# Optimization experiments

Measured on AMD Instinct MI355X. Metric: run time of the kernel, lower is better.

Reference implementation:

```python
import jax, jax.numpy as jnp
import numpy as np

EMBED = 768
HEADS = 12
HEAD_DIM = EMBED // HEADS
B, S = 1, 4096


def setup_inputs() -> dict:
    key = jax.random.key(0)
    ks = jax.random.split(key, 8)
    values = jax.random.normal(ks[0], (B, S, EMBED), dtype=jnp.float32)
    keys_in = jax.random.normal(ks[1], (B, S, EMBED), dtype=jnp.float32)
    queries = jax.random.normal(ks[2], (B, S, EMBED), dtype=jnp.float32)
    # causal mask: 1.0 where attention is disallowed (gets * -1e9)
    mask = jnp.triu(jnp.ones((S, S), dtype=jnp.float32), k=1)[None, None, :, :]
    sc = 1.0 / np.sqrt(EMBED)
    W_q = jax.random.normal(ks[3], (EMBED, EMBED), dtype=jnp.float32) * sc
    W_k = jax.random.normal(ks[4], (EMBED, EMBED), dtype=jnp.float32) * sc
    W_v = jax.random.normal(ks[5], (EMBED, EMBED), dtype=jnp.float32) * sc
    W_o = jax.random.normal(ks[6], (EMBED, EMBED), dtype=jnp.float32) * sc
    b_o = jnp.zeros((EMBED,), dtype=jnp.float32)
    return {"values": values, "keys": keys_in, "queries": queries, "mask": mask,
            "W_q": W_q, "W_k": W_k, "W_v": W_v, "W_o": W_o, "b_o": b_o}


def reference(values, keys, queries, mask, W_q, W_k, W_v, W_o, b_o):
    N, S_, _ = queries.shape
    # linear projections (Dense, no bias)
    q = queries @ W_q  # [N, S, E]
    k = keys @ W_k
    v = values @ W_v
    # split heads -> [N, H, S, Dh]
    def split(x):
        return x.reshape(N, S_, HEADS, HEAD_DIM).transpose(0, 2, 1, 3)
    q, k, v = split(q), split(k), split(v)
    scores = jnp.einsum('nhqd,nhkd->nhqk', q, k) / jnp.sqrt(
        jnp.asarray(HEAD_DIM, dtype=q.dtype))
    scores = scores + mask * (-1e9)
    attn = jax.nn.softmax(scores, axis=-1)
    out = jnp.einsum('nhqk,nhkd->nhqd', attn, v)  # [N, H, S, Dh]
    out = out.transpose(0, 2, 1, 3).reshape(N, S_, EMBED)
    return out @ W_o + b_o
```

## Files before the change

kernel.cpp:

```cpp
#include <hip/hip_runtime.h>

#define S_LEN 4096
#define EMB   768
#define NH    12
#define DH    64

typedef __attribute__((ext_vector_type(8))) short bf16x8;
typedef __attribute__((ext_vector_type(4))) float f32x4;

__device__ __forceinline__ unsigned short f2bf(float f) {
    union { float f; unsigned u; } v; v.f = f;
    unsigned r = v.u + 0x7fffu + ((v.u >> 16) & 1u);
    return (unsigned short)(r >> 16);
}
__device__ __forceinline__ float bf2f(unsigned short u) {
    union { unsigned u; float f; } v; v.u = (unsigned)u << 16; return v.f;
}
__device__ __forceinline__ unsigned pk2(float lo, float hi) {
    unsigned r;
    asm("v_cvt_pk_bf16_f32 %0, %1, %2" : "=v"(r) : "v"(lo), "v"(hi));
    return r;
}
__device__ __forceinline__ float fexp2(float x) {
    float r;
    asm("v_exp_f32 %0, %1" : "=v"(r) : "v"(x));
    return r;
}
__device__ __forceinline__ f32x4 mfma16(bf16x8 a, bf16x8 b, f32x4 c) {
    return __builtin_amdgcn_mfma_f32_16x16x32_bf16(a, b, c, 0, 0, 0);
}
__device__ __forceinline__ void async16(unsigned short* lds, const unsigned short* g) {
    __builtin_amdgcn_global_load_lds(
        (const __attribute__((address_space(1))) unsigned int*)(const void*)g,
        (__attribute__((address_space(3))) unsigned int*)(void*)lds, 16, 0, 0);
}

#define QSCALE 0.180336884f

__global__ __launch_bounds__(256) void prep(const float* __restrict__ Wq, const float* __restrict__ Wk,
                     const float* __restrict__ Wv, const float* __restrict__ Wo,
                     const float* __restrict__ q_in, const float* __restrict__ k_in,
                     const float* __restrict__ v_in,
                     unsigned short* __restrict__ WT, unsigned short* __restrict__ conv) {
    int bx = blockIdx.x, t = threadIdx.x;
    if (bx < 576) {
        __shared__ float tile[64][65];
        int z = bx / 144, rem = bx % 144;
        int k0 = (rem / 12) * 64, n0 = (rem % 12) * 64;
        const float* W = (z == 0) ? Wq : (z == 1) ? Wk : (z == 2) ? Wv : Wo;
        unsigned short* out = WT + (size_t)z * EMB * EMB;
        int row = t >> 2, c = (t & 3) * 16;
        const float4* src = (const float4*)(W + (size_t)(k0 + row) * EMB + n0 + c);
#pragma unroll
        for (int i = 0; i < 4; i++) {
            float4 v = src[i];
            tile[row][c + i * 4 + 0] = v.x; tile[row][c + i * 4 + 1] = v.y;
            tile[row][c + i * 4 + 2] = v.z; tile[row][c + i * 4 + 3] = v.w;
        }
        __syncthreads();
        unsigned short tmp[16] __attribute__((aligned(16)));
#pragma unroll
        for (int i = 0; i < 16; i++) tmp[i] = f2bf(tile[c + i][row]);
        int4* dst = (int4*)(out + (size_t)(n0 + row) * EMB + k0 + c);
        dst[0] = *(int4*)&tmp[0];
        dst[1] = *(int4*)&tmp[8];
    } else {
        size_t e8 = ((size_t)(bx - 576) * 256 + t) * 8;
        int z = (int)(e8 / 3145728);
        size_t off = e8 - (size_t)z * 3145728;
        const float* src = (z == 0) ? q_in : (z == 1) ? k_in : v_in;
        float4 a = *(const float4*)(src + off);
        float4 b = *(const float4*)(src + off + 4);
        unsigned r[4];
        r[0] = pk2(a.x, a.y); r[1] = pk2(a.z, a.w);
        r[2] = pk2(b.x, b.y); r[3] = pk2(b.z, b.w);
        *(int4*)(conv + e8) = *(int4*)r;
    }
}

__global__ __launch_bounds__(256) void gemm_qkv(const unsigned short* __restrict__ conv,
                                                const unsigned short* __restrict__ WT,
                                                unsigned short* __restrict__ Qh,
                                                unsigned short* __restrict__ Kh,
                                                unsigned short* __restrict__ Vt) {
    __shared__ unsigned short As[128 * 32];
    __shared__ unsigned short Bs[128 * 32];
    int m0 = blockIdx.x * 128;
    int z = blockIdx.y / 6, n0 = (blockIdx.y % 6) * 128;
    const unsigned short* A  = conv + (size_t)z * 3145728;
    const unsigned short* Bt = WT   + (size_t)z * 589824;
    int t = threadIdx.x, lane = t & 63, wv = t >> 6, quad = lane >> 4, l16 = lane & 15;
    int wm = wv >> 1, wn = wv & 1;
    int cfr = (quad ^ ((l16 >> 1) & 3)) * 8;

    const unsigned short* pa[2];
    const unsigned short* pb[2];
#pragma unroll
    for (int a2 = 0; a2 < 2; a2++) {
        int s1 = a2 * 256 + t, r = s1 >> 2, gc = (s1 & 3) ^ ((r >> 1) & 3);
        pa[a2] = A  + (size_t)(m0 + r) * EMB + gc * 8;
        pb[a2] = Bt + (size_t)(n0 + r) * EMB + gc * 8;
    }
    f32x4 acc[4][4] = {};

    for (int k0 = 0; k0 < EMB; k0 += 32) {
#pragma unroll
        for (int a2 = 0; a2 < 2; a2++) {
            async16(&As[(a2 * 256 + t) * 8], pa[a2] + k0);
            async16(&Bs[(a2 * 256 + t) * 8], pb[a2] + k0);
        }
        __syncthreads();
        bf16x8 fa[4], fb[4];
#pragma unroll
        for (int mi = 0; mi < 4; mi++)
            fa[mi] = *(bf16x8*)&As[(wm * 64 + mi * 16 + l16) * 32 + cfr];
#pragma unroll
        for (int ni = 0; ni < 4; ni++)
            fb[ni] = *(bf16x8*)&Bs[(wn * 64 + ni * 16 + l16) * 32 + cfr];
#pragma unroll
        for (int mi = 0; mi < 4; mi++)
#pragma unroll
            for (int ni = 0; ni < 4; ni++)
                acc[mi][ni] = mfma16(fa[mi], fb[ni], acc[mi][ni]);
        __syncthreads();
    }

    if (z == 2) {
#pragma unroll
        for (int mi = 0; mi < 4; mi++)
#pragma unroll
            for (int ni = 0; ni < 4; ni++) {
                int m = m0 + wm * 64 + mi * 16 + quad * 4;
                int n = n0 + wn * 64 + ni * 16 + l16;
                uint2 val;
                val.x = pk2(acc[mi][ni][0], acc[mi][ni][1]);
                val.y = pk2(acc[mi][ni][2], acc[mi][ni][3]);
                *(uint2*)&Vt[(size_t)(((n >> 6) << 6) + (n & 63)) * S_LEN + m] = val;
            }
    } else {
        unsigned short* dst = z ? Kh : Qh;
        float sc = z ? 1.0f : QSCALE;
#pragma unroll
        for (int mi = 0; mi < 4; mi++)
#pragma unroll
            for (int ni = 0; ni < 4; ni++)
#pragma unroll
                for (int r = 0; r < 4; r++) {
                    int m = m0 + wm * 64 + mi * 16 + quad * 4 + r;
                    int n = n0 + wn * 64 + ni * 16 + l16;
                    dst[((size_t)(n >> 6) * S_LEN + m) * 64 + (n & 63)] = f2bf(acc[mi][ni][r] * sc);
                }
    }
}

__global__ __launch_bounds__(256) void attn_kernel(const unsigned short* __restrict__ Qh,
                                                   const unsigned short* __restrict__ Kh,
                                                   const unsigned short* __restrict__ Vt,
                                                   unsigned short* __restrict__ Opart,
                                                   float* __restrict__ Lpart) {
    __shared__ unsigned short Kls[2][4096];
    __shared__ unsigned short Vls[2][4096];
    __shared__ unsigned short Pls[4 * 32 * 72];

    int p = blockIdx.x, h = blockIdx.y;
    int qb2 = 0, pre = 0;
    while (pre + (qb2 >> 2) + 1 <= p) { pre += (qb2 >> 2) + 1; qb2++; }
    int sp = p - pre;
    int part = h * 144 + p;
    int ntile = 2 * qb2 + 2;
    int jb = sp * 8, je = min(jb + 8, ntile);
    int q0 = qb2 << 7;

    int t = threadIdx.x, w = t >> 6, lane = t & 63, quad = lane >> 4, l16 = lane & 15;
    int rb = w * 32;
    int c0 = (quad ^ (l16 & 7)) * 8, c1 = (((quad + 4) ^ (l16 & 7))) * 8;

    const unsigned short* kb_ = Kh + (size_t)h * S_LEN * DH;
    const unsigned short* vb_ = Vt + (size_t)h * S_LEN * DH;

    bf16x8 aQ[2][2];
#pragma unroll
    for (int rg = 0; rg < 2; rg++)
#pragma unroll
        for (int kh = 0; kh < 2; kh++)
            aQ[rg][kh] = *(const bf16x8*)(Qh + ((size_t)h * S_LEN + q0 + rb + rg * 16 + l16) * 64 + kh * 32 + quad * 8);

    const unsigned short* pk_[2];
    const unsigned short* pv_[2];
    int ldso[2];
#pragma unroll
    for (int a2 = 0; a2 < 2; a2++) {
        int s1 = a2 * 256 + t, r = s1 >> 3, gc = (s1 & 7) ^ (r & 7);
        pk_[a2] = kb_ + (size_t)(jb * 64 + r) * 64 + gc * 8;
        pv_[a2] = vb_ + (size_t)r * S_LEN + jb * 64 + gc * 8;
        ldso[a2] = s1 * 8;
    }

    f32x4 o[4][2] = {};
    float lsum[2][4] = {};
    unsigned short* pwave = &Pls[w * 32 * 72];

#pragma unroll 1
    for (int jt = jb; jt < je; jt++) {
        int buf = (jt - jb) & 1;
        if (jt == jb) {
#pragma unroll
            for (int a2 = 0; a2 < 2; a2++) {
                async16(&Kls[0][ldso[a2]], pk_[a2]); pk_[a2] += 4096;
                async16(&Vls[0][ldso[a2]], pv_[a2]); pv_[a2] += 64;
            }
        }
        __syncthreads();
        if (jt + 1 < je) {
#pragma unroll
            for (int a2 = 0; a2 < 2; a2++) {
                async16(&Kls[buf ^ 1][ldso[a2]], pk_[a2]); pk_[a2] += 4096;
                async16(&Vls[buf ^ 1][ldso[a2]], pv_[a2]); pv_[a2] += 64;
            }
        }
        bool active = !(jt == 2 * qb2 + 1 && w < 2);
        if (active) {
            f32x4 s[2][4];
#pragma unroll
            for (int nt = 0; nt < 4; nt++) {
                int row = nt * 16 + l16;
                bf16x8 k0f = *(bf16x8*)&Kls[buf][row * 64 + c0];
                bf16x8 k1f = *(bf16x8*)&Kls[buf][row * 64 + c1];
#pragma unroll
                for (int rg = 0; rg < 2; rg++) {
                    f32x4 zz = {};
                    zz = mfma16(aQ[rg][0], k0f, zz);
                    zz = mfma16(aQ[rg][1], k1f, zz);
                    s[rg][nt] = zz;
                }
            }
            if (jt >= 2 * qb2) {
                int dlt = (jt - 2 * qb2) * 64;
#pragma unroll
                for (int rg = 0; rg < 2; rg++)
#pragma unroll
                    for (int nt = 0; nt < 4; nt++) {
                        int col = nt * 16 + l16;
#pragma unroll
                        for (int r = 0; r < 4; r++) {
                            int rel = rb + rg * 16 + quad * 4 + r - dlt;
                            if (col > rel) s[rg][nt][r] = -1e9f;
                        }
                    }
            }
#pragma unroll
            for (int rg = 0; rg < 2; rg++)
#pragma unroll
                for (int nt = 0; nt < 4; nt++) {
                    float p0 = fexp2(s[rg][nt][0]);
                    float p1 = fexp2(s[rg][nt][1]);
                    float p2 = fexp2(s[rg][nt][2]);
                    float p3 = fexp2(s[rg][nt][3]);
                    lsum[rg][0] += p0; lsum[rg][1] += p1;
                    lsum[rg][2] += p2; lsum[rg][3] += p3;
                    unsigned pa2 = pk2(p0, p1), pb2 = pk2(p2, p3);
                    unsigned short* pw = &pwave[(rg * 16 + quad * 4) * 72 + nt * 16 + l16];
                    pw[0]   = (unsigned short)pa2;
                    pw[72]  = (unsigned short)(pa2 >> 16);
                    pw[144] = (unsigned short)pb2;
                    pw[216] = (unsigned short)(pb2 >> 16);
                }
            asm volatile("s_waitcnt lgkmcnt(0)" ::: "memory");
            bf16x8 bP[2][2];
#pragma unroll
            for (int ntq = 0; ntq < 2; ntq++) {
                bP[ntq][0] = *(bf16x8*)&pwave[(ntq * 16 + l16) * 72 + quad * 8];
                bP[ntq][1] = *(bf16x8*)&pwave[(ntq * 16 + l16) * 72 + 32 + quad * 8];
            }
#pragma unroll
            for (int mt = 0; mt < 4; mt++) {
                int row = mt * 16 + l16;
                bf16x8 v0f = *(bf16x8*)&Vls[buf][row * 64 + c0];
                bf16x8 v1f = *(bf16x8*)&Vls[buf][row * 64 + c1];
#pragma unroll
                for (int ntq = 0; ntq < 2; ntq++) {
                    o[mt][ntq] = mfma16(v0f, bP[ntq][0], o[mt][ntq]);
                    o[mt][ntq] = mfma16(v1f, bP[ntq][1], o[mt][ntq]);
                }
            }
        }
    }

    unsigned short* op = Opart + (size_t)part * 8192;
#pragma unroll
    for (int mt = 0; mt < 4; mt++)
#pragma unroll
        for (int ntq = 0; ntq < 2; ntq++) {
            uint2 val;
            val.x = pk2(o[mt][ntq][0], o[mt][ntq][1]);
            val.y = pk2(o[mt][ntq][2], o[mt][ntq][3]);
            int q = rb + ntq * 16 + l16;
            int d = mt * 16 + quad * 4;
            *(uint2*)&op[q * 64 + d] = val;
        }
    float* lp = Lpart + (size_t)part * 128;
#pragma unroll
    for (int rg = 0; rg < 2; rg++)
#pragma unroll
        for (int r = 0; r < 4; r++) {
            float v = lsum[rg][r];
            v += __shfl_xor(v, 8); v += __shfl_xor(v, 4);
            v += __shfl_xor(v, 2); v += __shfl_xor(v, 1);
            if (l16 == 0) lp[rb + rg * 16 + quad * 4 + r] = v;
        }
}

__global__ __launch_bounds__(256) void merge(const unsigned short* __restrict__ Opart,
                                             const float* __restrict__ Lpart,
                                             unsigned short* __restrict__ O) {
    int qb2 = blockIdx.x, h = blockIdx.y;
    int a = qb2 >> 2, b = qb2 & 3;
    int pre = qb2 + 2 * a * (a - 1) + a * b;
    int cnt = a + 1;
    int pbase = h * 144 + pre;
    int t = threadIdx.x, row = t >> 1, ch = (t & 1) * 32;

    float acc[32] = {};
    float ls = 0.f;
    const unsigned short* src = Opart + (size_t)pbase * 8192 + row * 64 + ch;
    for (int p2 = 0; p2 < cnt; p2++) {
        ls += Lpart[(size_t)(pbase + p2) * 128 + row];
        const int4* s4 = (const int4*)(src + (size_t)p2 * 8192);
#pragma unroll
        for (int i = 0; i < 4; i++) {
            int4 x = s4[i];
            const unsigned short* xs = (const unsigned short*)&x;
#pragma unroll
            for (int j = 0; j < 8; j++) acc[i * 8 + j] += bf2f(xs[j]);
        }
    }
    float inv = 1.0f / ls;
    unsigned outp[16];
#pragma unroll
    for (int i = 0; i < 16; i++) outp[i] = pk2(acc[2 * i] * inv, acc[2 * i + 1] * inv);
    int4* dst = (int4*)(O + (size_t)(qb2 * 128 + row) * EMB + h * 64 + ch);
#pragma unroll
    for (int i = 0; i < 4; i++) dst[i] = *(int4*)&outp[i * 4];
}

__global__ __launch_bounds__(256) void gemm_out(const unsigned short* __restrict__ O,
                                                const unsigned short* __restrict__ WT,
                                                const float* __restrict__ bias,
                                                float* __restrict__ out) {
    __shared__ unsigned short As[128 * 32];
    __shared__ unsigned short Bs[64 * 32];
    int m0 = blockIdx.x * 128, n0 = blockIdx.y * 64;
    const unsigned short* Bt = WT + (size_t)3 * 589824;
    int t = threadIdx.x, lane = t & 63, wv = t >> 6, quad = lane >> 4, l16 = lane & 15;
    int wm = wv >> 1, wn = wv & 1;
    int cfr = (quad ^ ((l16 >> 1) & 3)) * 8;

    const unsigned short* pa[2];
    const unsigned short* pb;
#pragma unroll
    for (int a2 = 0; a2 < 2; a2++) {
        int s1 = a2 * 256 + t, r = s1 >> 2, gc = (s1 & 3) ^ ((r >> 1) & 3);
        pa[a2] = O + (size_t)(m0 + r) * EMB + gc * 8;
    }
    {
        int r = t >> 2, gc = (t & 3) ^ ((r >> 1) & 3);
        pb = Bt + (size_t)(n0 + r) * EMB + gc * 8;
    }
    f32x4 acc[4][2] = {};

    for (int k0 = 0; k0 < EMB; k0 += 32) {
#pragma unroll
        for (int a2 = 0; a2 < 2; a2++)
            async16(&As[(a2 * 256 + t) * 8], pa[a2] + k0);
        async16(&Bs[t * 8], pb + k0);
        __syncthreads();
        bf16x8 fa[4], fb[2];
#pragma unroll
        for (int mi = 0; mi < 4; mi++)
            fa[mi] = *(bf16x8*)&As[(wm * 64 + mi * 16 + l16) * 32 + cfr];
#pragma unroll
        for (int ni = 0; ni < 2; ni++)
            fb[ni] = *(bf16x8*)&Bs[(wn * 32 + ni * 16 + l16) * 32 + cfr];
#pragma unroll
        for (int mi = 0; mi < 4; mi++)
#pragma unroll
            for (int ni = 0; ni < 2; ni++)
                acc[mi][ni] = mfma16(fa[mi], fb[ni], acc[mi][ni]);
        __syncthreads();
    }

    float bv[2];
#pragma unroll
    for (int ni = 0; ni < 2; ni++) bv[ni] = bias[n0 + wn * 32 + ni * 16 + l16];
#pragma unroll
    for (int mi = 0; mi < 4; mi++)
#pragma unroll
        for (int ni = 0; ni < 2; ni++)
#pragma unroll
            for (int r = 0; r < 4; r++) {
                int m = m0 + wm * 64 + mi * 16 + quad * 4 + r;
                int n = n0 + wn * 32 + ni * 16 + l16;
                out[(size_t)m * EMB + n] = acc[mi][ni][r] + bv[ni];
            }
}

extern "C" void kernel_launch(void* const* d_in, const int* in_sizes, int n_in,
                              void* d_out, int out_size, void* d_ws, size_t ws_size,
                              hipStream_t stream) {
    const float* values  = (const float*)d_in[0];
    const float* keys    = (const float*)d_in[1];
    const float* queries = (const float*)d_in[2];
    const float* Wq = (const float*)d_in[4];
    const float* Wk = (const float*)d_in[5];
    const float* Wv = (const float*)d_in[6];
    const float* Wo = (const float*)d_in[7];
    const float* bo = (const float*)d_in[8];

    char* ws = (char*)d_ws;
    unsigned short* WT = (unsigned short*)ws;
    unsigned short* Qh = (unsigned short*)(ws + 4718592);
    unsigned short* Kh = (unsigned short*)(ws + 11010048);
    unsigned short* Vt = (unsigned short*)(ws + 17301504);
    unsigned short* O  = (unsigned short*)(ws + 23592960);
    unsigned short* conv = (unsigned short*)(ws + 29884416);
    unsigned short* Op   = (unsigned short*)(ws + 29884416);
    float*          Lp   = (float*)(ws + 29884416 + 28311552);
    float* out = (float*)d_out;

    prep<<<dim3(5184), 256, 0, stream>>>(Wq, Wk, Wv, Wo, queries, keys, values, WT, conv);
    gemm_qkv<<<dim3(32, 18), 256, 0, stream>>>(conv, WT, Qh, Kh, Vt);
    attn_kernel<<<dim3(144, 12), 256, 0, stream>>>(Qh, Kh, Vt, Op, Lp);
    merge<<<dim3(32, 12), 256, 0, stream>>>(Op, Lp, O);
    gemm_out<<<dim3(32, 12), 256, 0, stream>>>(O, WT, bo, out);
}
```

Before: 252.4 us.

## Fuse fp32-to-bf16 input conversion into QKV GEMM and read K/V directly from global

Drops the separate activation-conversion pass in prep: gemm_qkv now loads fp32 rows straight from global memory into registers and packs them to bf16 for the A fragments. Separately, the attention kernel no longer stages K and V tiles through double-buffered LDS with async loads and barriers, and instead has each wave load its MFMA fragments directly from global memory, relying on cache hits. This removes one full read/write of the inputs and the per-tile barriers, at the cost of uncoalesced per-lane global loads, redundant K/V fetches across the four waves, and no prefetch overlap in the attention loop.

Result: slower. 363.8 us (+44.1%).

```diff
diff --git a/kernel.cpp b/kernel.cpp
--- a/kernel.cpp
+++ b/kernel.cpp
@@ -39,81 +39,73 @@
 
 __global__ __launch_bounds__(256) void prep(const float* __restrict__ Wq, const float* __restrict__ Wk,
                      const float* __restrict__ Wv, const float* __restrict__ Wo,
-                     const float* __restrict__ q_in, const float* __restrict__ k_in,
-                     const float* __restrict__ v_in,
-                     unsigned short* __restrict__ WT, unsigned short* __restrict__ conv) {
+                     unsigned short* __restrict__ WT) {
+    __shared__ float tile[64][65];
     int bx = blockIdx.x, t = threadIdx.x;
-    if (bx < 576) {
-        __shared__ float tile[64][65];
-        int z = bx / 144, rem = bx % 144;
-        int k0 = (rem / 12) * 64, n0 = (rem % 12) * 64;
-        const float* W = (z == 0) ? Wq : (z == 1) ? Wk : (z == 2) ? Wv : Wo;
-        unsigned short* out = WT + (size_t)z * EMB * EMB;
-        int row = t >> 2, c = (t & 3) * 16;
-        const float4* src = (const float4*)(W + (size_t)(k0 + row) * EMB + n0 + c);
-#pragma unroll
-        for (int i = 0; i < 4; i++) {
-            float4 v = src[i];
-            tile[row][c + i * 4 + 0] = v.x; tile[row][c + i * 4 + 1] = v.y;
-            tile[row][c + i * 4 + 2] = v.z; tile[row][c + i * 4 + 3] = v.w;
-        }
-        __syncthreads();
-        unsigned short tmp[16] __attribute__((aligned(16)));
-#pragma unroll
-        for (int i = 0; i < 16; i++) tmp[i] = f2bf(tile[c + i][row]);
-        int4* dst = (int4*)(out + (size_t)(n0 + row) * EMB + k0 + c);
-        dst[0] = *(int4*)&tmp[0];
-        dst[1] = *(int4*)&tmp[8];
-    } else {
-        size_t e8 = ((size_t)(bx - 576) * 256 + t) * 8;
-        int z = (int)(e8 / 3145728);
-        size_t off = e8 - (size_t)z * 3145728;
-        const float* src = (z == 0) ? q_in : (z == 1) ? k_in : v_in;
-        float4 a = *(const float4*)(src + off);
-        float4 b = *(const float4*)(src + off + 4);
-        unsigned r[4];
-        r[0] = pk2(a.x, a.y); r[1] = pk2(a.z, a.w);
-        r[2] = pk2(b.x, b.y); r[3] = pk2(b.z, b.w);
-        *(int4*)(conv + e8) = *(int4*)r;
-    }
-}
-
-__global__ __launch_bounds__(256) void gemm_qkv(const unsigned short* __restrict__ conv,
+    int z = bx / 144, rem = bx % 144;
+    int k0 = (rem / 12) * 64, n0 = (rem % 12) * 64;
+    const float* W = (z == 0) ? Wq : (z == 1) ? Wk : (z == 2) ? Wv : Wo;
+    unsigned short* out = WT + (size_t)z * EMB * EMB;
+    int row = t >> 2, c = (t & 3) * 16;
+    const float4* src = (const float4*)(W + (size_t)(k0 + row) * EMB + n0 + c);
+#pragma unroll
+    for (int i = 0; i < 4; i++) {
+        float4 v = src[i];
+        tile[row][c + i * 4 + 0] = v.x; tile[row][c + i * 4 + 1] = v.y;
+        tile[row][c + i * 4 + 2] = v.z; tile[row][c + i * 4 + 3] = v.w;
+    }
+    __syncthreads();
+    unsigned short tmp[16] __attribute__((aligned(16)));
+#pragma unroll
+    for (int i = 0; i < 16; i++) tmp[i] = f2bf(tile[c + i][row]);
+    int4* dst = (int4*)(out + (size_t)(n0 + row) * EMB + k0 + c);
+    dst[0] = *(int4*)&tmp[0];
+    dst[1] = *(int4*)&tmp[8];
+}
+
+__global__ __launch_bounds__(256) void gemm_qkv(const float* __restrict__ Aq,
+                                                const float* __restrict__ Ak,
+                                                const float* __restrict__ Av,
                                                 const unsigned short* __restrict__ WT,
                                                 unsigned short* __restrict__ Qh,
                                                 unsigned short* __restrict__ Kh,
                                                 unsigned short* __restrict__ Vt) {
-    __shared__ unsigned short As[128 * 32];
     __shared__ unsigned short Bs[128 * 32];
     int m0 = blockIdx.x * 128;
     int z = blockIdx.y / 6, n0 = (blockIdx.y % 6) * 128;
-    const unsigned short* A  = conv + (size_t)z * 3145728;
-    const unsigned short* Bt = WT   + (size_t)z * 589824;
+    const float* A = (z == 0) ? Aq : (z == 1) ? Ak : Av;
+    const unsigned short* Bt = WT + (size_t)z * 589824;
     int t = threadIdx.x, lane = t & 63, wv = t >> 6, quad = lane >> 4, l16 = lane & 15;
     int wm = wv >> 1, wn = wv & 1;
     int cfr = (quad ^ ((l16 >> 1) & 3)) * 8;
 
-    const unsigned short* pa[2];
+    const float* gaf = A + (size_t)(m0 + wm * 64 + l16) * EMB + quad * 8;
+
     const unsigned short* pb[2];
 #pragma unroll
     for (int a2 = 0; a2 < 2; a2++) {
         int s1 = a2 * 256 + t, r = s1 >> 2, gc = (s1 & 3) ^ ((r >> 1) & 3);
-        pa[a2] = A  + (size_t)(m0 + r) * EMB + gc * 8;
         pb[a2] = Bt + (size_t)(n0 + r) * EMB + gc * 8;
     }
     f32x4 acc[4][4] = {};
 
     for (int k0 = 0; k0 < EMB; k0 += 32) {
 #pragma unroll
-        for (int a2 = 0; a2 < 2; a2++) {
-            async16(&As[(a2 * 256 + t) * 8], pa[a2] + k0);
+        for (int a2 = 0; a2 < 2; a2++)
             async16(&Bs[(a2 * 256 + t) * 8], pb[a2] + k0);
+        bf16x8 fa[4];
+#pragma unroll
+        for (int mi = 0; mi < 4; mi++) {
+            const float* gp = gaf + (size_t)(mi * 16) * EMB + k0;
+            float4 x0 = *(const float4*)gp;
+            float4 x1 = *(const float4*)(gp + 4);
+            unsigned b[4];
+            b[0] = pk2(x0.x, x0.y); b[1] = pk2(x0.z, x0.w);
+            b[2] = pk2(x1.x, x1.y); b[3] = pk2(x1.z, x1.w);
+            fa[mi] = *(bf16x8*)b;
         }
         __syncthreads();
-        bf16x8 fa[4], fb[4];
-#pragma unroll
-        for (int mi = 0; mi < 4; mi++)
-            fa[mi] = *(bf16x8*)&As[(wm * 64 + mi * 16 + l16) * 32 + cfr];
+        bf16x8 fb[4];
 #pragma unroll
         for (int ni = 0; ni < 4; ni++)
             fb[ni] = *(bf16x8*)&Bs[(wn * 64 + ni * 16 + l16) * 32 + cfr];
@@ -158,8 +150,6 @@
                                                    const unsigned short* __restrict__ Vt,
                                                    unsigned short* __restrict__ Opart,
                                                    float* __restrict__ Lpart) {
-    __shared__ unsigned short Kls[2][4096];
-    __shared__ unsigned short Vls[2][4096];
     __shared__ unsigned short Pls[4 * 32 * 72];
 
     int p = blockIdx.x, h = blockIdx.y;
@@ -173,10 +163,9 @@
 
     int t = threadIdx.x, w = t >> 6, lane = t & 63, quad = lane >> 4, l16 = lane & 15;
     int rb = w * 32;
-    int c0 = (quad ^ (l16 & 7)) * 8, c1 = (((quad + 4) ^ (l16 & 7))) * 8;
-
-    const unsigned short* kb_ = Kh + (size_t)h * S_LEN * DH;
-    const unsigned short* vb_ = Vt + (size_t)h * S_LEN * DH;
+
+    const unsigned short* kb_ = Kh + (size_t)h * S_LEN * DH + l16 * 64 + quad * 8;
+    const unsigned short* vb_ = Vt + ((size_t)h * DH + l16) * S_LEN + quad * 8;
 
     bf16x8 aQ[2][2];
 #pragma unroll
@@ -184,17 +173,6 @@
 #pragma unroll
         for (int kh = 0; kh < 2; kh++)
             aQ[rg][kh] = *(const bf16x8*)(Qh + ((size_t)h * S_LEN + q0 + rb + rg * 16 + l16) * 64 + kh * 32 + quad * 8);
-
-    const unsigned short* pk_[2];
-    const unsigned short* pv_[2];
-    int ldso[2];
-#pragma unroll
-    for (int a2 = 0; a2 < 2; a2++) {
-        int s1 = a2 * 256 + t, r = s1 >> 3, gc = (s1 & 7) ^ (r & 7);
-        pk_[a2] = kb_ + (size_t)(jb * 64 + r) * 64 + gc * 8;
-        pv_[a2] = vb_ + (size_t)r * S_LEN + jb * 64 + gc * 8;
-        ldso[a2] = s1 * 8;
-    }
 
     f32x4 o[4][2] = {};
     float lsum[2][4] = {};
@@ -202,87 +180,70 @@
 
 #pragma unroll 1
     for (int jt = jb; jt < je; jt++) {
-        int buf = (jt - jb) & 1;
-        if (jt == jb) {
-#pragma unroll
-            for (int a2 = 0; a2 < 2; a2++) {
-                async16(&Kls[0][ldso[a2]], pk_[a2]); pk_[a2] += 4096;
-                async16(&Vls[0][ldso[a2]], pv_[a2]); pv_[a2] += 64;
+        if (jt == 2 * qb2 + 1 && w < 2) continue;
+        int j0 = jt * 64;
+
+        f32x4 s[2][4];
+#pragma unroll
+        for (int nt = 0; nt < 4; nt++) {
+            const unsigned short* kp = kb_ + (size_t)(j0 + nt * 16) * 64;
+            bf16x8 k0f = *(const bf16x8*)kp;
+            bf16x8 k1f = *(const bf16x8*)(kp + 32);
+#pragma unroll
+            for (int rg = 0; rg < 2; rg++) {
+                f32x4 zz = {};
+                zz = mfma16(aQ[rg][0], k0f, zz);
+                zz = mfma16(aQ[rg][1], k1f, zz);
+                s[rg][nt] = zz;
             }
         }
-        __syncthreads();
-        if (jt + 1 < je) {
-#pragma unroll
-            for (int a2 = 0; a2 < 2; a2++) {
-                async16(&Kls[buf ^ 1][ldso[a2]], pk_[a2]); pk_[a2] += 4096;
-                async16(&Vls[buf ^ 1][ldso[a2]], pv_[a2]); pv_[a2] += 64;
+        if (jt >= 2 * qb2) {
+            int dlt = (jt - 2 * qb2) * 64;
+#pragma unroll
+            for (int rg = 0; rg < 2; rg++)
+#pragma unroll
+                for (int nt = 0; nt < 4; nt++) {
+                    int col = nt * 16 + l16;
+#pragma unroll
+                    for (int r = 0; r < 4; r++) {
+                        int rel = rb + rg * 16 + quad * 4 + r - dlt;
+                        if (col > rel) s[rg][nt][r] = -1e9f;
+                    }
+                }
+        }
+#pragma unroll
+        for (int rg = 0; rg < 2; rg++)
+#pragma unroll
+            for (int nt = 0; nt < 4; nt++) {
+                float p0 = fexp2(s[rg][nt][0]);
+                float p1 = fexp2(s[rg][nt][1]);
+                float p2 = fexp2(s[rg][nt][2]);
+                float p3 = fexp2(s[rg][nt][3]);
+                lsum[rg][0] += p0; lsum[rg][1] += p1;
+                lsum[rg][2] += p2; lsum[rg][3] += p3;
+                unsigned pa2 = pk2(p0, p1), pb2 = pk2(p2, p3);
+                unsigned short* pw = &pwave[(rg * 16 + quad * 4) * 72 + nt * 16 + l16];
+                pw[0]   = (unsigned short)pa2;
+                pw[72]  = (unsigned short)(pa2 >> 16);
+                pw[144] = (unsigned short)pb2;
+                pw[216] = (unsigned short)(pb2 >> 16);
             }
-        }
-        bool active = !(jt == 2 * qb2 + 1 && w < 2);
-        if (active) {
-            f32x4 s[2][4];
-#pragma unroll
-            for (int nt = 0; nt < 4; nt++) {
-                int row = nt * 16 + l16;
-                bf16x8 k0f = *(bf16x8*)&Kls[buf][row * 64 + c0];
-                bf16x8 k1f = *(bf16x8*)&Kls[buf][row * 64 + c1];
-#pragma unroll
-                for (int rg = 0; rg < 2; rg++) {
-                    f32x4 zz = {};
-                    zz = mfma16(aQ[rg][0], k0f, zz);
-                    zz = mfma16(aQ[rg][1], k1f, zz);
-                    s[rg][nt] = zz;
-                }
-            }
-            if (jt >= 2 * qb2) {
-                int dlt = (jt - 2 * qb2) * 64;
-#pragma unroll
-                for (int rg = 0; rg < 2; rg++)
-#pragma unroll
-                    for (int nt = 0; nt < 4; nt++) {
-                        int col = nt * 16 + l16;
-#pragma unroll
-                        for (int r = 0; r < 4; r++) {
-                            int rel = rb + rg * 16 + quad * 4 + r - dlt;
-                            if (col > rel) s[rg][nt][r] = -1e9f;
-                        }
-                    }
-            }
-#pragma unroll
-            for (int rg = 0; rg < 2; rg++)
-#pragma unroll
-                for (int nt = 0; nt < 4; nt++) {
-                    float p0 = fexp2(s[rg][nt][0]);
-                    float p1 = fexp2(s[rg][nt][1]);
-                    float p2 = fexp2(s[rg][nt][2]);
-                    float p3 = fexp2(s[rg][nt][3]);
-                    lsum[rg][0] += p0; lsum[rg][1] += p1;
-                    lsum[rg][2] += p2; lsum[rg][3] += p3;
-                    unsigned pa2 = pk2(p0, p1), pb2 = pk2(p2, p3);
-                    unsigned short* pw = &pwave[(rg * 16 + quad * 4) * 72 + nt * 16 + l16];
-                    pw[0]   = (unsigned short)pa2;
-                    pw[72]  = (unsigned short)(pa2 >> 16);
-                    pw[144] = (unsigned short)pb2;
-                    pw[216] = (unsigned short)(pb2 >> 16);
-                }
-            asm volatile("s_waitcnt lgkmcnt(0)" ::: "memory");
-            bf16x8 bP[2][2];
-#pragma unroll
-            for (int ntq = 0; ntq < 2; ntq++) {
-                bP[ntq][0] = *(bf16x8*)&pwave[(ntq * 16 + l16) * 72 + quad * 8];
-                bP[ntq][1] = *(bf16x8*)&pwave[(ntq * 16 + l16) * 72 + 32 + quad * 8];
-            }
-#pragma unroll
-            for (int mt = 0; mt < 4; mt++) {
-                int row = mt * 16 + l16;
-                bf16x8 v0f = *(bf16x8*)&Vls[buf][row * 64 + c0];
-                bf16x8 v1f = *(bf16x8*)&Vls[buf][row * 64 + c1];
-#pragma unroll
-                for (int ntq = 0; ntq < 2; ntq++) {
-                    o[mt][ntq] = mfma16(v0f, bP[ntq][0], o[mt][ntq]);
-                    o[mt][ntq] = mfma16(v1f, bP[ntq][1], o[mt][ntq]);
-                }
-            }
+        asm volatile("s_waitcnt lgkmcnt(0)" ::: "memory");
+        bf16x8 bP[2][2];
+#pragma unroll
+        for (int ntq = 0; ntq < 2; ntq++) {
+            bP[ntq][0] = *(bf16x8*)&pwave[(ntq * 16 + l16) * 72 + quad * 8];
+            bP[ntq][1] = *(bf16x8*)&pwave[(ntq * 16 + l16) * 72 + 32 + quad * 8];
+        }
+#pragma unroll
+        for (int mt = 0; mt < 4; mt++) {
+            const unsigned short* vp = vb_ + (size_t)(mt * 16) * S_LEN + j0;
+            bf16x8 v0f = *(const bf16x8*)vp;
+            bf16x8 v1f = *(const bf16x8*)(vp + 32);
+            o[mt][0] = mfma16(v0f, bP[0][0], o[mt][0]);
+            o[mt][0] = mfma16(v1f, bP[0][1], o[mt][0]);
+            o[mt][1] = mfma16(v0f, bP[1][0], o[mt][1]);
+            o[mt][1] = mfma16(v1f, bP[1][1], o[mt][1]);
         }
     }
 
@@ -422,13 +383,12 @@
     unsigned short* Kh = (unsigned short*)(ws + 11010048);
     unsigned short* Vt = (unsigned short*)(ws + 17301504);
     unsigned short* O  = (unsigned short*)(ws + 23592960);
-    unsigned short* conv = (unsigned short*)(ws + 29884416);
-    unsigned short* Op   = (unsigned short*)(ws + 29884416);
-    float*          Lp   = (float*)(ws + 29884416 + 28311552);
+    unsigned short* Op = (unsigned short*)(ws + 29884416);
+    float*          Lp = (float*)(ws + 29884416 + 28311552);
     float* out = (float*)d_out;
 
-    prep<<<dim3(5184), 256, 0, stream>>>(Wq, Wk, Wv, Wo, queries, keys, values, WT, conv);
-    gemm_qkv<<<dim3(32, 18), 256, 0, stream>>>(conv, WT, Qh, Kh, Vt);
+    prep<<<dim3(576), 256, 0, stream>>>(Wq, Wk, Wv, Wo, WT);
+    gemm_qkv<<<dim3(32, 18), 256, 0, stream>>>(queries, keys, values, WT, Qh, Kh, Vt);
     attn_kernel<<<dim3(144, 12), 256, 0, stream>>>(Qh, Kh, Vt, Op, Lp);
     merge<<<dim3(32, 12), 256, 0, stream>>>(Op, Lp, O);
     gemm_out<<<dim3(32, 12), 256, 0, stream>>>(O, WT, bo, out);
```

## Shrink GEMM tiles for more blocks and transpose QK^T MFMA for row-wise P stores

Applied to the files above, without the earlier changes.

The QKV and output-projection GEMMs now use 64-row M tiles, which doubles their grid size so more of the GPU's compute units are occupied. In the attention kernel the QK^T MFMA operands are swapped so each lane holds a query row's scores. The causal mask and row sums become per-lane, P is written to shared memory as packed 8-byte stores instead of scalar 16-bit stores, and the row-sum reduction needs only two shuffles. The smaller GEMM tiles lower per-block data reuse and add extra global loads of the weight tiles.

Measured after the change: 245.0 us. -2.9%, faster.

```diff
diff --git a/kernel.cpp b/kernel.cpp
--- a/kernel.cpp
+++ b/kernel.cpp
@@ -83,44 +83,43 @@
                                                 unsigned short* __restrict__ Qh,
                                                 unsigned short* __restrict__ Kh,
                                                 unsigned short* __restrict__ Vt) {
-    __shared__ unsigned short As[128 * 32];
+    __shared__ unsigned short As[64 * 32];
     __shared__ unsigned short Bs[128 * 32];
-    int m0 = blockIdx.x * 128;
+    int m0 = blockIdx.x * 64;
     int z = blockIdx.y / 6, n0 = (blockIdx.y % 6) * 128;
     const unsigned short* A  = conv + (size_t)z * 3145728;
     const unsigned short* Bt = WT   + (size_t)z * 589824;
     int t = threadIdx.x, lane = t & 63, wv = t >> 6, quad = lane >> 4, l16 = lane & 15;
-    int wm = wv >> 1, wn = wv & 1;
+    int wn = wv;
     int cfr = (quad ^ ((l16 >> 1) & 3)) * 8;
 
-    const unsigned short* pa[2];
+    int rA = t >> 2, gcA = (t & 3) ^ ((rA >> 1) & 3);
+    const unsigned short* pa = A + (size_t)(m0 + rA) * EMB + gcA * 8;
     const unsigned short* pb[2];
 #pragma unroll
     for (int a2 = 0; a2 < 2; a2++) {
-        int s1 = a2 * 256 + t, r = s1 >> 2, gc = (s1 & 3) ^ ((r >> 1) & 3);
-        pa[a2] = A  + (size_t)(m0 + r) * EMB + gc * 8;
-        pb[a2] = Bt + (size_t)(n0 + r) * EMB + gc * 8;
-    }
-    f32x4 acc[4][4] = {};
+        int s1 = a2 * 256 + t, rB = s1 >> 2, gcB = (s1 & 3) ^ ((rB >> 1) & 3);
+        pb[a2] = Bt + (size_t)(n0 + rB) * EMB + gcB * 8;
+    }
+    f32x4 acc[4][2] = {};
 
     for (int k0 = 0; k0 < EMB; k0 += 32) {
-#pragma unroll
-        for (int a2 = 0; a2 < 2; a2++) {
-            async16(&As[(a2 * 256 + t) * 8], pa[a2] + k0);
+        async16(&As[t * 8], pa + k0);
+#pragma unroll
+        for (int a2 = 0; a2 < 2; a2++)
             async16(&Bs[(a2 * 256 + t) * 8], pb[a2] + k0);
-        }
-        __syncthreads();
-        bf16x8 fa[4], fb[4];
+        __syncthreads();
+        bf16x8 fa[4], fb[2];
 #pragma unroll
         for (int mi = 0; mi < 4; mi++)
-            fa[mi] = *(bf16x8*)&As[(wm * 64 + mi * 16 + l16) * 32 + cfr];
-#pragma unroll
-        for (int ni = 0; ni < 4; ni++)
-            fb[ni] = *(bf16x8*)&Bs[(wn * 64 + ni * 16 + l16) * 32 + cfr];
+            fa[mi] = *(bf16x8*)&As[(mi * 16 + l16) * 32 + cfr];
+#pragma unroll
+        for (int ni = 0; ni < 2; ni++)
+            fb[ni] = *(bf16x8*)&Bs[(wn * 32 + ni * 16 + l16) * 32 + cfr];
 #pragma unroll
         for (int mi = 0; mi < 4; mi++)
 #pragma unroll
-            for (int ni = 0; ni < 4; ni++)
+            for (int ni = 0; ni < 2; ni++)
                 acc[mi][ni] = mfma16(fa[mi], fb[ni], acc[mi][ni]);
         __syncthreads();
     }
@@ -129,9 +128,9 @@
 #pragma unroll
         for (int mi = 0; mi < 4; mi++)
 #pragma unroll
-            for (int ni = 0; ni < 4; ni++) {
-                int m = m0 + wm * 64 + mi * 16 + quad * 4;
-                int n = n0 + wn * 64 + ni * 16 + l16;
+            for (int ni = 0; ni < 2; ni++) {
+                int m = m0 + mi * 16 + quad * 4;
+                int n = n0 + wn * 32 + ni * 16 + l16;
                 uint2 val;
                 val.x = pk2(acc[mi][ni][0], acc[mi][ni][1]);
                 val.y = pk2(acc[mi][ni][2], acc[mi][ni][3]);
@@ -143,11 +142,11 @@
 #pragma unroll
         for (int mi = 0; mi < 4; mi++)
 #pragma unroll
-            for (int ni = 0; ni < 4; ni++)
+            for (int ni = 0; ni < 2; ni++)
 #pragma unroll
                 for (int r = 0; r < 4; r++) {
-                    int m = m0 + wm * 64 + mi * 16 + quad * 4 + r;
-                    int n = n0 + wn * 64 + ni * 16 + l16;
+                    int m = m0 + mi * 16 + quad * 4 + r;
+                    int n = n0 + wn * 32 + ni * 16 + l16;
                     dst[((size_t)(n >> 6) * S_LEN + m) * 64 + (n & 63)] = f2bf(acc[mi][ni][r] * sc);
                 }
     }
@@ -197,7 +196,7 @@
     }
 
     f32x4 o[4][2] = {};
-    float lsum[2][4] = {};
+    float lsum[2] = {0.f, 0.f};
     unsigned short* pwave = &Pls[w * 32 * 72];
 
 #pragma unroll 1
@@ -229,24 +228,22 @@
 #pragma unroll
                 for (int rg = 0; rg < 2; rg++) {
                     f32x4 zz = {};
-                    zz = mfma16(aQ[rg][0], k0f, zz);
-                    zz = mfma16(aQ[rg][1], k1f, zz);
+                    zz = mfma16(k0f, aQ[rg][0], zz);
+                    zz = mfma16(k1f, aQ[rg][1], zz);
                     s[rg][nt] = zz;
                 }
             }
             if (jt >= 2 * qb2) {
                 int dlt = (jt - 2 * qb2) * 64;
 #pragma unroll
-                for (int rg = 0; rg < 2; rg++)
-#pragma unroll
-                    for (int nt = 0; nt < 4; nt++) {
-                        int col = nt * 16 + l16;
-#pragma unroll
-                        for (int r = 0; r < 4; r++) {
-                            int rel = rb + rg * 16 + quad * 4 + r - dlt;
-                            if (col > rel) s[rg][nt][r] = -1e9f;
-                        }
-                    }
+                for (int rg = 0; rg < 2; rg++) {
+                    int qrel = rb + rg * 16 + l16 - dlt;
+#pragma unroll
+                    for (int nt = 0; nt < 4; nt++)
+#pragma unroll
+                        for (int r = 0; r < 4; r++)
+                            if (nt * 16 + quad * 4 + r > qrel) s[rg][nt][r] = -1e9f;
+                }
             }
 #pragma unroll
             for (int rg = 0; rg < 2; rg++)
@@ -256,14 +253,11 @@
                     float p1 = fexp2(s[rg][nt][1]);
                     float p2 = fexp2(s[rg][nt][2]);
                     float p3 = fexp2(s[rg][nt][3]);
-                    lsum[rg][0] += p0; lsum[rg][1] += p1;
-                    lsum[rg][2] += p2; lsum[rg][3] += p3;
-                    unsigned pa2 = pk2(p0, p1), pb2 = pk2(p2, p3);
-                    unsigned short* pw = &pwave[(rg * 16 + quad * 4) * 72 + nt * 16 + l16];
-                    pw[0]   = (unsigned short)pa2;
-                    pw[72]  = (unsigned short)(pa2 >> 16);
-                    pw[144] = (unsigned short)pb2;
-                    pw[216] = (unsigned short)(pb2 >> 16);
+                    lsum[rg] += (p0 + p1) + (p2 + p3);
+                    uint2 val;
+                    val.x = pk2(p0, p1);
+                    val.y = pk2(p2, p3);
+                    *(uint2*)&pwave[(rg * 16 + l16) * 72 + nt * 16 + quad * 4] = val;
                 }
             asm volatile("s_waitcnt lgkmcnt(0)" ::: "memory");
             bf16x8 bP[2][2];
@@ -300,14 +294,11 @@
         }
     float* lp = Lpart + (size_t)part * 128;
 #pragma unroll
-    for (int rg = 0; rg < 2; rg++)
-#pragma unroll
-        for (int r = 0; r < 4; r++) {
-            float v = lsum[rg][r];
-            v += __shfl_xor(v, 8); v += __shfl_xor(v, 4);
-            v += __shfl_xor(v, 2); v += __shfl_xor(v, 1);
-            if (l16 == 0) lp[rb + rg * 16 + quad * 4 + r] = v;
-        }
+    for (int rg = 0; rg < 2; rg++) {
+        float v = lsum[rg];
+        v += __shfl_xor(v, 16); v += __shfl_xor(v, 32);
+        if (quad == 0) lp[rb + rg * 16 + l16] = v;
+    }
 }
 
 __global__ __launch_bounds__(256) void merge(const unsigned short* __restrict__ Opart,
@@ -347,42 +338,32 @@
                                                 const unsigned short* __restrict__ WT,
                                                 const float* __restrict__ bias,
                                                 float* __restrict__ out) {
-    __shared__ unsigned short As[128 * 32];
+    __shared__ unsigned short As[64 * 32];
     __shared__ unsigned short Bs[64 * 32];
-    int m0 = blockIdx.x * 128, n0 = blockIdx.y * 64;
+    int m0 = blockIdx.x * 64, n0 = blockIdx.y * 64;
     const unsigned short* Bt = WT + (size_t)3 * 589824;
     int t = threadIdx.x, lane = t & 63, wv = t >> 6, quad = lane >> 4, l16 = lane & 15;
     int wm = wv >> 1, wn = wv & 1;
     int cfr = (quad ^ ((l16 >> 1) & 3)) * 8;
 
-    const unsigned short* pa[2];
-    const unsigned short* pb;
-#pragma unroll
-    for (int a2 = 0; a2 < 2; a2++) {
-        int s1 = a2 * 256 + t, r = s1 >> 2, gc = (s1 & 3) ^ ((r >> 1) & 3);
-        pa[a2] = O + (size_t)(m0 + r) * EMB + gc * 8;
-    }
-    {
-        int r = t >> 2, gc = (t & 3) ^ ((r >> 1) & 3);
-        pb = Bt + (size_t)(n0 + r) * EMB + gc * 8;
-    }
-    f32x4 acc[4][2] = {};
+    int rA = t >> 2, gcA = (t & 3) ^ ((rA >> 1) & 3);
+    const unsigned short* pa = O  + (size_t)(m0 + rA) * EMB + gcA * 8;
+    const unsigned short* pb = Bt + (size_t)(n0 + rA) * EMB + gcA * 8;
+    f32x4 acc[2][2] = {};
 
     for (int k0 = 0; k0 < EMB; k0 += 32) {
-#pragma unroll
-        for (int a2 = 0; a2 < 2; a2++)
-            async16(&As[(a2 * 256 + t) * 8], pa[a2] + k0);
+        async16(&As[t * 8], pa + k0);
         async16(&Bs[t * 8], pb + k0);
         __syncthreads();
-        bf16x8 fa[4], fb[2];
-#pragma unroll
-        for (int mi = 0; mi < 4; mi++)
-            fa[mi] = *(bf16x8*)&As[(wm * 64 + mi * 16 + l16) * 32 + cfr];
+        bf16x8 fa[2], fb[2];
+#pragma unroll
+        for (int mi = 0; mi < 2; mi++)
+            fa[mi] = *(bf16x8*)&As[(wm * 32 + mi * 16 + l16) * 32 + cfr];
 #pragma unroll
         for (int ni = 0; ni < 2; ni++)
             fb[ni] = *(bf16x8*)&Bs[(wn * 32 + ni * 16 + l16) * 32 + cfr];
 #pragma unroll
-        for (int mi = 0; mi < 4; mi++)
+        for (int mi = 0; mi < 2; mi++)
 #pragma unroll
             for (int ni = 0; ni < 2; ni++)
                 acc[mi][ni] = mfma16(fa[mi], fb[ni], acc[mi][ni]);
@@ -393,12 +374,12 @@
 #pragma unroll
     for (int ni = 0; ni < 2; ni++) bv[ni] = bias[n0 + wn * 32 + ni * 16 + l16];
 #pragma unroll
-    for (int mi = 0; mi < 4; mi++)
+    for (int mi = 0; mi < 2; mi++)
 #pragma unroll
         for (int ni = 0; ni < 2; ni++)
 #pragma unroll
             for (int r = 0; r < 4; r++) {
-                int m = m0 + wm * 64 + mi * 16 + quad * 4 + r;
+                int m = m0 + wm * 32 + mi * 16 + quad * 4 + r;
                 int n = n0 + wn * 32 + ni * 16 + l16;
                 out[(size_t)m * EMB + n] = acc[mi][ni][r] + bv[ni];
             }
@@ -428,8 +409,8 @@
     float* out = (float*)d_out;
 
     prep<<<dim3(5184), 256, 0, stream>>>(Wq, Wk, Wv, Wo, queries, keys, values, WT, conv);
-    gemm_qkv<<<dim3(32, 18), 256, 0, stream>>>(conv, WT, Qh, Kh, Vt);
+    gemm_qkv<<<dim3(64, 18), 256, 0, stream>>>(conv, WT, Qh, Kh, Vt);
     attn_kernel<<<dim3(144, 12), 256, 0, stream>>>(Qh, Kh, Vt, Op, Lp);
     merge<<<dim3(32, 12), 256, 0, stream>>>(Op, Lp, O);
-    gemm_out<<<dim3(32, 12), 256, 0, stream>>>(O, WT, bo, out);
-}
+    gemm_out<<<dim3(64, 12), 256, 0, stream>>>(O, WT, bo, out);
+}
```
